# Kernel tuning notes

Measured on AMD Instinct MI355X. Metric: run time of the kernel, lower is better.

The kernel has to match this reference:

```python
import jax, jax.numpy as jnp
import numpy as np

B, N = 1, 4096
D_IN, D_OUT, H = 256, 256, 8
HD = D_OUT // H
NEG = -9e15


def _xavier(key, shape):
    lim = np.sqrt(6.0 / (shape[0] + shape[1])).astype(np.float32)
    return jax.random.uniform(key, shape, jnp.float32, -lim, lim)


def setup_inputs() -> dict:
    key = jax.random.key(0)
    ks = jax.random.split(key, 8)
    x = jax.random.normal(ks[0], (B, N, D_IN), jnp.float32)
    adj = (jax.random.uniform(ks[1], (B, N, N)) < 0.05).astype(jnp.float32)
    idx = jnp.arange(N)
    adj = adj.at[:, idx, idx].set(1.0)
    Wq = _xavier(ks[2], (D_IN, D_OUT)); bq = jnp.zeros((D_OUT,), jnp.float32)
    Wk = _xavier(ks[3], (D_IN, D_OUT)); bk = jnp.zeros((D_OUT,), jnp.float32)
    Wv = _xavier(ks[4], (D_IN, D_OUT)); bv = jnp.zeros((D_OUT,), jnp.float32)
    Wo = _xavier(ks[5], (D_OUT, D_OUT)); bo = jnp.zeros((D_OUT,), jnp.float32)
    return dict(x=x, adj=adj, Wq=Wq, bq=bq, Wk=Wk, bk=bk, Wv=Wv, bv=bv, Wo=Wo, bo=bo)


def reference(x, adj, Wq, bq, Wk, bk, Wv, bv, Wo, bo):
    b, n, _ = x.shape
    def split_heads(t):  # [B,N,D_OUT] -> [B,H,N,HD]
        return t.reshape(b, n, H, HD).transpose(0, 2, 1, 3)
    q = split_heads(x @ Wq + bq)
    k = split_heads(x @ Wk + bk)
    v = split_heads(x @ Wv + bv)
    scores = jnp.einsum('bhqd,bhkd->bhqk', q, k) / np.float32(np.sqrt(HD))
    scores = jnp.where(adj[:, None, :, :] > 0, scores, jnp.float32(NEG))
    attn = jax.nn.softmax(scores, axis=-1)
    # dropout is identity in eval mode (training=False)
    out = jnp.einsum('bhqk,bhkd->bhqd', attn, v)
    out = out.transpose(0, 2, 1, 3).reshape(b, n, D_OUT)
    return out @ Wo + bo
```

## Files before the change

### kernel.cpp

```cpp
#include <hip/hip_runtime.h>
#include <hip/hip_bf16.h>
#include <stdint.h>

#define NTOK 4096
#define DIM  256
#define NH   8
#define HD   32
#define MAXNNZ 512

typedef __attribute__((ext_vector_type(8))) short short8;
typedef __attribute__((ext_vector_type(4))) float float4v;
typedef unsigned short u16;
typedef unsigned int u32;

__device__ __forceinline__ float bf2f(u16 u) {
    union { u32 u; float f; } c; c.u = ((u32)u) << 16; return c.f;
}
__device__ __forceinline__ u16 f2bf(float f) {
    union { float f; u32 u; } c; c.f = f;
    u32 u = c.u;
    u = u + 0x7FFFu + ((u >> 16) & 1u);
    return (u16)(u >> 16);
}
__device__ __forceinline__ float blo(u32 c) {
    union { u32 u; float f; } x; x.u = c << 16; return x.f;
}
__device__ __forceinline__ float bhi(u32 c) {
    union { u32 u; float f; } x; x.u = c & 0xFFFF0000u; return x.f;
}

__global__ void x_to_bf16(const float* __restrict__ x, u16* __restrict__ xb) {
    int i = (blockIdx.x * blockDim.x + threadIdx.x) * 4;
    float4 v = *(const float4*)(x + i);
    ushort4 o;
    o.x = f2bf(v.x); o.y = f2bf(v.y); o.z = f2bf(v.z); o.w = f2bf(v.w);
    *(ushort4*)(xb + i) = o;
}

__global__ void transpose_w(const float* __restrict__ Wq, const float* __restrict__ Wk,
                            const float* __restrict__ Wv, const float* __restrict__ Wo,
                            u16* __restrict__ WT) {
    const float* srcs[4] = {Wq, Wk, Wv, Wo};
    const float* W = srcs[blockIdx.y];
    int o = blockIdx.x, i = threadIdx.x;
    WT[blockIdx.y * 65536 + o * 256 + i] = f2bf(W[i * 256 + o]);
}

__global__ __launch_bounds__(256) void adj_to_list(const float* __restrict__ adj,
                                                   u16* __restrict__ NL,
                                                   u32* __restrict__ NC) {
    __shared__ u32 cnt;
    int row = blockIdx.x, t = threadIdx.x;
    if (t == 0) cnt = 0;
    __syncthreads();
    const float4* rp = (const float4*)(adj + (size_t)row * NTOK);
    u16* lbase = NL + (size_t)row * MAXNNZ;
#pragma unroll
    for (int i = 0; i < 4; ++i) {
        float4 v = rp[i * 256 + t];
        u32 m = 0;
        if (v.x != 0.f) m |= 1u;
        if (v.y != 0.f) m |= 2u;
        if (v.z != 0.f) m |= 4u;
        if (v.w != 0.f) m |= 8u;
        if (m) {
            int p = __popc(m);
            u32 base = atomicAdd(&cnt, (u32)p);
            int col0 = (i * 256 + t) * 4;
            while (m) {
                int j = __builtin_ctz(m);
                m &= m - 1;
                if (base < MAXNNZ) lbase[base] = (u16)(col0 + j);
                ++base;
            }
        }
    }
    __syncthreads();
    if (t == 0) NC[row] = (cnt < MAXNNZ) ? cnt : MAXNNZ;
}

__global__ __launch_bounds__(64) void qkv_gemm(
    const u16* __restrict__ xb,
    const u16* __restrict__ WT,
    const float* __restrict__ bq, const float* __restrict__ bk, const float* __restrict__ bv,
    u16* __restrict__ Q, u16* __restrict__ K, u16* __restrict__ V) {
    int lane = threadIdx.x, quad = lane >> 4, l16 = lane & 15;
    int mtile = blockIdx.x, ntile = blockIdx.y, mat = blockIdx.z;
    const float* bias = (mat == 0) ? bq : (mat == 1) ? bk : bv;
    const u16* arow = xb + (size_t)(mtile * 16 + l16) * DIM + quad * 8;
    const u16* brow = WT + (size_t)mat * 65536 + (size_t)(ntile * 16 + l16) * DIM + quad * 8;
    float4v acc = {0.f, 0.f, 0.f, 0.f};
#pragma unroll
    for (int k0 = 0; k0 < DIM; k0 += 32) {
        short8 af = *(const short8*)(arow + k0);
        short8 bf = *(const short8*)(brow + k0);
        acc = __builtin_amdgcn_mfma_f32_16x16x32_bf16(af, bf, acc, 0, 0, 0);
    }
    int n = ntile * 16 + l16;
    float bb = bias[n];
    const float sc = (mat == 0) ? 0.25503635559913516f : 1.0f;
    u16* dst = (mat == 0) ? Q : (mat == 1) ? K : V;
#pragma unroll
    for (int r = 0; r < 4; ++r) {
        int m = mtile * 16 + quad * 4 + r;
        dst[(size_t)m * DIM + n] = f2bf((acc[r] + bb) * sc);
    }
}

__global__ __launch_bounds__(256, 8) void sparse_attn(
    const u16* __restrict__ Q, const u16* __restrict__ K, const u16* __restrict__ V,
    const u16* __restrict__ NL, const u32* __restrict__ NC,
    u16* __restrict__ AO) {
    __shared__ float part[2][32][9];
    int tid  = threadIdx.x;
    int rb   = tid >> 7;
    int half = (tid >> 6) & 1;
    int lane = tid & 63;
    int p = lane >> 5;
    int t = lane & 31;
    int row = blockIdx.x * 2 + rb;

    uint4 qq = *(const uint4*)(Q + (size_t)row * DIM + t * 8);
    float q0 = blo(qq.x), q1 = bhi(qq.x), q2 = blo(qq.y), q3 = bhi(qq.y);
    float q4 = blo(qq.z), q5 = bhi(qq.z), q6 = blo(qq.w), q7 = bhi(qq.w);

    float O[8];
#pragma unroll
    for (int i = 0; i < 8; ++i) O[i] = 0.f;
    float lsum = 0.f;

    int nnz = (int)NC[row];
    const u16* lst = NL + (size_t)row * MAXNNZ;
    int nh    = ((nnz + 4) >> 3) << 2;
    int begin = half ? nh : 0;
    int end   = half ? nnz : nh;
    const u16* Kt = K + t * 8;
    const u16* Vt = V + t * 8;

#define PAIR_BODY(kk, vv, e_valid)                                               \
    {                                                                            \
        float a = 0.f, b = 0.f;                                                  \
        a = fmaf(blo(kk.x), q0, a); b = fmaf(bhi(kk.x), q1, b);                  \
        a = fmaf(blo(kk.y), q2, a); b = fmaf(bhi(kk.y), q3, b);                  \
        a = fmaf(blo(kk.z), q4, a); b = fmaf(bhi(kk.z), q5, b);                  \
        a = fmaf(blo(kk.w), q6, a); b = fmaf(bhi(kk.w), q7, b);                  \
        float s = a + b;                                                         \
        s += __shfl_xor(s, 1, 64);                                               \
        s += __shfl_xor(s, 2, 64);      \
        float e = __builtin_amdgcn_exp2f(s);                                     \
        e = (e_valid) ? e : 0.f;                                                 \
        lsum += e;                                                               \
        O[0] = fmaf(e, blo(vv.x), O[0]); O[1] = fmaf(e, bhi(vv.x), O[1]);        \
        O[2] = fmaf(e, blo(vv.y), O[2]); O[3] = fmaf(e, bhi(vv.y), O[3]);        \
        O[4] = fmaf(e, blo(vv.z), O[4]); O[5] = fmaf(e, bhi(vv.z), O[5]);        \
        O[6] = fmaf(e, blo(vv.w), O[6]); O[7] = fmaf(e, bhi(vv.w), O[7]);        \
    }

    if (begin < end) {
        u32 wA = *(const u32*)(lst + begin);
        u32 wB = (begin + 2 < end) ? *(const u32*)(lst + begin + 2) : wA;
        for (int i2 = begin; i2 < end; i2 += 4) {
            bool vA = (i2 + p) < end;
            bool vB = (i2 + 2 + p) < end;
            int lo = (int)(wA & 0xFFFFu);
            int iA = p ? (int)(wA >> 16) : lo;
            int iB = p ? (int)(wB >> 16) : (int)(wB & 0xFFFFu);
            if (!vA) iA = lo;
            if (!vB) iB = lo;

            int in0 = i2 + 4, in2 = i2 + 6;
            u32 wAn = *(const u32*)(lst + ((in0 < end) ? in0 : begin));
            u32 wBn = *(const u32*)(lst + ((in2 < end) ? in2 : begin));

            uint4 kA  = *(const uint4*)(Kt + (size_t)iA * DIM);
            uint4 vAv = *(const uint4*)(Vt + (size_t)iA * DIM);
            uint4 kB  = *(const uint4*)(Kt + (size_t)iB * DIM);
            uint4 vBv = *(const uint4*)(Vt + (size_t)iB * DIM);

            PAIR_BODY(kA, vAv, vA)
            PAIR_BODY(kB, vBv, vB)

            wA = wAn; wB = wBn;
        }
    }
#undef PAIR_BODY

#pragma unroll
    for (int i = 0; i < 8; ++i) O[i] += __shfl_xor(O[i], 32, 64);
    lsum += __shfl_xor(lsum, 32, 64);

    if (half == 1 && p == 0) {
#pragma unroll
        for (int i = 0; i < 8; ++i) part[rb][t][i] = O[i];
        part[rb][t][8] = lsum;
    }
    __syncthreads();
    if (half == 0 && p == 0) {
#pragma unroll
        for (int i = 0; i < 8; ++i) O[i] += part[rb][t][i];
        lsum += part[rb][t][8];
        float inv = 1.0f / lsum;
        u32 w0 = (u32)f2bf(O[0] * inv) | ((u32)f2bf(O[1] * inv) << 16);
        u32 w1 = (u32)f2bf(O[2] * inv) | ((u32)f2bf(O[3] * inv) << 16);
        u32 w2 = (u32)f2bf(O[4] * inv) | ((u32)f2bf(O[5] * inv) << 16);
        u32 w3 = (u32)f2bf(O[6] * inv) | ((u32)f2bf(O[7] * inv) << 16);
        *(uint4*)(AO + (size_t)row * DIM + t * 8) = make_uint4(w0, w1, w2, w3);
    }
}

__global__ __launch_bounds__(64) void out_gemm(
    const u16* __restrict__ AO, const u16* __restrict__ WTo, const float* __restrict__ bo,
    float* __restrict__ out) {
    int lane = threadIdx.x, quad = lane >> 4, l16 = lane & 15;
    int mtile = blockIdx.x, ntile = blockIdx.y;
    const u16* arow = AO + (size_t)(mtile * 16 + l16) * DIM + quad * 8;
    const u16* brow = WTo + (size_t)(ntile * 16 + l16) * DIM + quad * 8;
    float4v acc = {0.f, 0.f, 0.f, 0.f};
#pragma unroll
    for (int k0 = 0; k0 < DIM; k0 += 32) {
        short8 af = *(const short8*)(arow + k0);
        short8 bf = *(const short8*)(brow + k0);
        acc = __builtin_amdgcn_mfma_f32_16x16x32_bf16(af, bf, acc, 0, 0, 0);
    }
    int n = ntile * 16 + l16;
    float bb = bo[n];
#pragma unroll
    for (int r = 0; r < 4; ++r)
        out[(size_t)(mtile * 16 + quad * 4 + r) * DIM + n] = acc[r] + bb;
}

extern "C" void kernel_launch(void* const* d_in, const int* in_sizes, int n_in,
                              void* d_out, int out_size, void* d_ws, size_t ws_size,
                              hipStream_t stream) {
    const float* x   = (const float*)d_in[0];
    const float* adj = (const float*)d_in[1];
    const float* Wq  = (const float*)d_in[2];
    const float* bq  = (const float*)d_in[3];
    const float* Wk  = (const float*)d_in[4];
    const float* bk  = (const float*)d_in[5];
    const float* Wv  = (const float*)d_in[6];
    const float* bv  = (const float*)d_in[7];
    const float* Wo  = (const float*)d_in[8];
    const float* bo  = (const float*)d_in[9];

    char* ws = (char*)d_ws;
    const size_t MB = 1u << 20;
    u16* Q   = (u16*)(ws);
    u16* K   = (u16*)(ws + 2 * MB);
    u16* V   = (u16*)(ws + 4 * MB);
    u16* AO  = (u16*)(ws + 6 * MB);
    u16* WT  = (u16*)(ws + 8 * MB);
    u16* XB  = (u16*)(ws + 8 * MB + 512 * 1024);
    u16* NL  = (u16*)(ws + 11 * MB);
    u32* NC  = (u32*)(ws + 15 * MB);

    x_to_bf16<<<dim3(1024), 256, 0, stream>>>(x, XB);
    transpose_w<<<dim3(256, 4), 256, 0, stream>>>(Wq, Wk, Wv, Wo, WT);
    adj_to_list<<<dim3(4096), 256, 0, stream>>>(adj, NL, NC);
    qkv_gemm<<<dim3(256, 16, 3), 64, 0, stream>>>(XB, WT, bq, bk, bv, Q, K, V);
    sparse_attn<<<dim3(2048), 256, 0, stream>>>(Q, K, V, NL, NC, AO);
    out_gemm<<<dim3(256, 16), 64, 0, stream>>>(AO, WT + 3 * 65536, bo, (float*)d_out);
}
```

Before: 197.0 us.

## Store Q/K in fp16 and use fdot2, packed FMA, and uniform loop bounds

Q and K are now written in fp16 so the sparse attention score dot product can use v_dot2 (fdot2) instead of eight scalar FMAs. The V accumulation uses 2-wide float vectors, which can map to packed FMA. Row, nnz and bounds are made wave-uniform with readfirstlane, and the main loop is split into an unmasked steady state plus a masked tail. Index math becomes 32-bit offsets. Together these cut ALU and address work in the gather loop, at the cost of fp16 range and precision for Q and K.

```diff
diff --git a/kernel.cpp b/kernel.cpp
--- a/kernel.cpp
+++ b/kernel.cpp
@@ -10,6 +10,8 @@
 
 typedef __attribute__((ext_vector_type(8))) short short8;
 typedef __attribute__((ext_vector_type(4))) float float4v;
+typedef __attribute__((ext_vector_type(2))) float f32x2;
+typedef __attribute__((ext_vector_type(2))) _Float16 h2;
 typedef unsigned short u16;
 typedef unsigned int u32;
 
@@ -21,6 +23,12 @@
     u32 u = c.u;
     u = u + 0x7FFFu + ((u >> 16) & 1u);
     return (u16)(u >> 16);
+}
+__device__ __forceinline__ u16 f2h(float f) {
+    union { _Float16 h; u16 u; } c; c.h = (_Float16)f; return c.u;
+}
+__device__ __forceinline__ h2 bch2(u32 v) {
+    union { u32 u; h2 h; } c; c.u = v; return c.h;
 }
 __device__ __forceinline__ float blo(u32 c) {
     union { u32 u; float f; } x; x.u = c << 16; return x.f;
@@ -103,7 +111,8 @@
 #pragma unroll
     for (int r = 0; r < 4; ++r) {
         int m = mtile * 16 + quad * 4 + r;
-        dst[(size_t)m * DIM + n] = f2bf((acc[r] + bb) * sc);
+        float y = (acc[r] + bb) * sc;
+        dst[(size_t)m * DIM + n] = (mat == 2) ? f2bf(y) : f2h(y);
     }
 }
 
@@ -113,97 +122,101 @@
     u16* __restrict__ AO) {
     __shared__ float part[2][32][9];
     int tid  = threadIdx.x;
-    int rb   = tid >> 7;
-    int half = (tid >> 6) & 1;
+    int rb   = __builtin_amdgcn_readfirstlane(tid >> 7);
+    int half = __builtin_amdgcn_readfirstlane((tid >> 6) & 1);
     int lane = tid & 63;
     int p = lane >> 5;
     int t = lane & 31;
-    int row = blockIdx.x * 2 + rb;
+    int row = __builtin_amdgcn_readfirstlane((int)blockIdx.x * 2 + rb);
+    int pshift = p << 4;
+    u32 tOff = (u32)(t * 8);
 
     uint4 qq = *(const uint4*)(Q + (size_t)row * DIM + t * 8);
-    float q0 = blo(qq.x), q1 = bhi(qq.x), q2 = blo(qq.y), q3 = bhi(qq.y);
-    float q4 = blo(qq.z), q5 = bhi(qq.z), q6 = blo(qq.w), q7 = bhi(qq.w);
-
-    float O[8];
-#pragma unroll
-    for (int i = 0; i < 8; ++i) O[i] = 0.f;
+    h2 qh0 = bch2(qq.x), qh1 = bch2(qq.y), qh2 = bch2(qq.z), qh3 = bch2(qq.w);
+
+    f32x2 O0 = {0.f, 0.f}, O1 = {0.f, 0.f}, O2 = {0.f, 0.f}, O3 = {0.f, 0.f};
     float lsum = 0.f;
 
-    int nnz = (int)NC[row];
+    int nnz = __builtin_amdgcn_readfirstlane((int)NC[row]);
     const u16* lst = NL + (size_t)row * MAXNNZ;
     int nh    = ((nnz + 4) >> 3) << 2;
     int begin = half ? nh : 0;
     int end   = half ? nnz : nh;
-    const u16* Kt = K + t * 8;
-    const u16* Vt = V + t * 8;
-
-#define PAIR_BODY(kk, vv, e_valid)                                               \
+
+#define BODY(kk, vv, EVALID)                                                     \
     {                                                                            \
-        float a = 0.f, b = 0.f;                                                  \
-        a = fmaf(blo(kk.x), q0, a); b = fmaf(bhi(kk.x), q1, b);                  \
-        a = fmaf(blo(kk.y), q2, a); b = fmaf(bhi(kk.y), q3, b);                  \
-        a = fmaf(blo(kk.z), q4, a); b = fmaf(bhi(kk.z), q5, b);                  \
-        a = fmaf(blo(kk.w), q6, a); b = fmaf(bhi(kk.w), q7, b);                  \
+        float a = __builtin_amdgcn_fdot2(bch2(kk.x), qh0, 0.f, false);           \
+        float b = __builtin_amdgcn_fdot2(bch2(kk.y), qh1, 0.f, false);           \
+        a = __builtin_amdgcn_fdot2(bch2(kk.z), qh2, a, false);                   \
+        b = __builtin_amdgcn_fdot2(bch2(kk.w), qh3, b, false);                   \
         float s = a + b;                                                         \
         s += __shfl_xor(s, 1, 64);                                               \
         s += __shfl_xor(s, 2, 64);      \
         float e = __builtin_amdgcn_exp2f(s);                                     \
-        e = (e_valid) ? e : 0.f;                                                 \
+        if (!(EVALID)) e = 0.f;                 \
         lsum += e;                                                               \
-        O[0] = fmaf(e, blo(vv.x), O[0]); O[1] = fmaf(e, bhi(vv.x), O[1]);        \
-        O[2] = fmaf(e, blo(vv.y), O[2]); O[3] = fmaf(e, bhi(vv.y), O[3]);        \
-        O[4] = fmaf(e, blo(vv.z), O[4]); O[5] = fmaf(e, bhi(vv.z), O[5]);        \
-        O[6] = fmaf(e, blo(vv.w), O[6]); O[7] = fmaf(e, bhi(vv.w), O[7]);        \
+        f32x2 ev = {e, e};                                                       \
+        O0 = __builtin_elementwise_fma(ev, (f32x2){blo(vv.x), bhi(vv.x)}, O0);   \
+        O1 = __builtin_elementwise_fma(ev, (f32x2){blo(vv.y), bhi(vv.y)}, O1);   \
+        O2 = __builtin_elementwise_fma(ev, (f32x2){blo(vv.z), bhi(vv.z)}, O2);   \
+        O3 = __builtin_elementwise_fma(ev, (f32x2){blo(vv.w), bhi(vv.w)}, O3);   \
     }
 
     if (begin < end) {
         u32 wA = *(const u32*)(lst + begin);
-        u32 wB = (begin + 2 < end) ? *(const u32*)(lst + begin + 2) : wA;
-        for (int i2 = begin; i2 < end; i2 += 4) {
-            bool vA = (i2 + p) < end;
-            bool vB = (i2 + 2 + p) < end;
-            int lo = (int)(wA & 0xFFFFu);
-            int iA = p ? (int)(wA >> 16) : lo;
-            int iB = p ? (int)(wB >> 16) : (int)(wB & 0xFFFFu);
-            if (!vA) iA = lo;
-            if (!vB) iB = lo;
-
-            int in0 = i2 + 4, in2 = i2 + 6;
-            u32 wAn = *(const u32*)(lst + ((in0 < end) ? in0 : begin));
-            u32 wBn = *(const u32*)(lst + ((in2 < end) ? in2 : begin));
-
-            uint4 kA  = *(const uint4*)(Kt + (size_t)iA * DIM);
-            uint4 vAv = *(const uint4*)(Vt + (size_t)iA * DIM);
-            uint4 kB  = *(const uint4*)(Kt + (size_t)iB * DIM);
-            uint4 vBv = *(const uint4*)(Vt + (size_t)iB * DIM);
-
-            PAIR_BODY(kA, vAv, vA)
-            PAIR_BODY(kB, vBv, vB)
-
+        u32 wB = *(const u32*)(lst + begin + 2);
+        int i2 = begin;
+        for (; i2 + 4 <= end; i2 += 4) {
+            u32 offA = (((wA >> pshift) & 0xFFFFu) << 8) + tOff;
+            u32 offB = (((wB >> pshift) & 0xFFFFu) << 8) + tOff;
+            u32 wAn = *(const u32*)(lst + i2 + 4);
+            u32 wBn = *(const u32*)(lst + i2 + 6);
+            uint4 kA  = *(const uint4*)(K + offA);
+            uint4 vAv = *(const uint4*)(V + offA);
+            uint4 kB  = *(const uint4*)(K + offB);
+            uint4 vBv = *(const uint4*)(V + offB);
+            BODY(kA, vAv, true)
+            BODY(kB, vBv, true)
             wA = wAn; wB = wBn;
         }
-    }
-#undef PAIR_BODY
-
-#pragma unroll
-    for (int i = 0; i < 8; ++i) O[i] += __shfl_xor(O[i], 32, 64);
+        if (i2 < end) {
+            u32 lo = wA & 0xFFFFu;
+            bool mA = (i2 + p) < end;
+            bool mB = (i2 + 2 + p) < end;
+            u32 idxA = mA ? ((wA >> pshift) & 0xFFFFu) : lo;
+            u32 idxB = mB ? ((wB >> pshift) & 0xFFFFu) : lo;
+            u32 offA = (idxA << 8) + tOff;
+            u32 offB = (idxB << 8) + tOff;
+            uint4 kA  = *(const uint4*)(K + offA);
+            uint4 vAv = *(const uint4*)(V + offA);
+            uint4 kB  = *(const uint4*)(K + offB);
+            uint4 vBv = *(const uint4*)(V + offB);
+            BODY(kA, vAv, mA)
+            BODY(kB, vBv, mB)
+        }
+    }
+#undef BODY
+
+    float Of[8] = {O0.x, O0.y, O1.x, O1.y, O2.x, O2.y, O3.x, O3.y};
+#pragma unroll
+    for (int i = 0; i < 8; ++i) Of[i] += __shfl_xor(Of[i], 32, 64);
     lsum += __shfl_xor(lsum, 32, 64);
 
     if (half == 1 && p == 0) {
 #pragma unroll
-        for (int i = 0; i < 8; ++i) part[rb][t][i] = O[i];
+        for (int i = 0; i < 8; ++i) part[rb][t][i] = Of[i];
         part[rb][t][8] = lsum;
     }
     __syncthreads();
     if (half == 0 && p == 0) {
 #pragma unroll
-        for (int i = 0; i < 8; ++i) O[i] += part[rb][t][i];
+        for (int i = 0; i < 8; ++i) Of[i] += part[rb][t][i];
         lsum += part[rb][t][8];
         float inv = 1.0f / lsum;
-        u32 w0 = (u32)f2bf(O[0] * inv) | ((u32)f2bf(O[1] * inv) << 16);
-        u32 w1 = (u32)f2bf(O[2] * inv) | ((u32)f2bf(O[3] * inv) << 16);
-        u32 w2 = (u32)f2bf(O[4] * inv) | ((u32)f2bf(O[5] * inv) << 16);
-        u32 w3 = (u32)f2bf(O[6] * inv) | ((u32)f2bf(O[7] * inv) << 16);
+        u32 w0 = (u32)f2bf(Of[0] * inv) | ((u32)f2bf(Of[1] * inv) << 16);
+        u32 w1 = (u32)f2bf(Of[2] * inv) | ((u32)f2bf(Of[3] * inv) << 16);
+        u32 w2 = (u32)f2bf(Of[4] * inv) | ((u32)f2bf(Of[5] * inv) << 16);
+        u32 w3 = (u32)f2bf(Of[6] * inv) | ((u32)f2bf(Of[7] * inv) << 16);
         *(uint4*)(AO + (size_t)row * DIM + t * 8) = make_uint4(w0, w1, w2, w3);
     }
 }
```

Result: faster. 190.5 us (-3.3%).
